# Kernel optimization log

Hardware: AMD Instinct MI355X
Metric: run time of the kernel (lower is better)

Reference implementation:

```python
import jax, jax.numpy as jnp
import numpy as np

HEADS = 4
DIM_HEAD = 32


def setup_inputs() -> dict:
    key = jax.random.key(0)
    k1, k2, k3 = jax.random.split(key, 3)
    B, L, D = 16, 8192, 256
    hidden = HEADS * DIM_HEAD  # 128
    x = jax.random.normal(k1, (B, L, D), dtype=jnp.float32)
    W_qkv = jax.random.normal(k2, (D, 3 * hidden), dtype=jnp.float32) * (D ** -0.5)
    W_out = jax.random.normal(k3, (hidden, D), dtype=jnp.float32) * (hidden ** -0.5)
    b_out = jnp.zeros((D,), dtype=jnp.float32)
    return {"x": x, "W_qkv": W_qkv, "W_out": W_out, "b_out": b_out}


def reference(x, W_qkv, W_out, b_out):
    B, L, D = x.shape
    scale = DIM_HEAD ** -0.5
    # 1x1 conv == per-token matmul
    qkv = jnp.einsum('bld,df->blf', x, W_qkv)  # [B, L, 3*h*dh]
    qkv = qkv.reshape(B, L, 3, HEADS, DIM_HEAD)
    q = jnp.transpose(qkv[:, :, 0], (0, 2, 1, 3)) * scale          # [B, h, L, d]
    k = jax.nn.softmax(jnp.transpose(qkv[:, :, 1], (0, 2, 1, 3)), axis=2)  # softmax over L
    v = jnp.transpose(qkv[:, :, 2], (0, 2, 1, 3))                  # [B, h, L, e]
    context = jnp.einsum('bhld,bhle->bhde', k, v)                  # [B, h, d, e]
    out = jnp.einsum('bhde,bhld->bhle', context, q)                # [B, h, L, e]
    out = jnp.transpose(out, (0, 2, 1, 3)).reshape(B, L, HEADS * DIM_HEAD)
    return jnp.einsum('blf,fd->bld', out, W_out) + b_out
```

## Files before the change

kernel.cpp:

```cpp
#include <hip/hip_runtime.h>
#include <math.h>


#define BL 131072

typedef __attribute__((ext_vector_type(8))) short bf16x8;
typedef __attribute__((ext_vector_type(4))) float f32x4;
typedef __attribute__((ext_vector_type(4))) unsigned u32x4;

__device__ __forceinline__ unsigned cvt_pk2(float a, float b) {
    unsigned r;
    asm("v_cvt_pk_bf16_f32 %0, %1, %2" : "=v"(r) : "v"(a), "v"(b));
    return r;
}
__device__ __forceinline__ ushort bf16_rn(float f) {
    return (ushort)cvt_pk2(f, f);
}
__device__ __forceinline__ float bf16f(ushort h) { return __uint_as_float(((unsigned)h) << 16); }

__device__ __forceinline__ void glds16(const void* g, void* l) {
    __builtin_amdgcn_global_load_lds((const __attribute__((address_space(1))) unsigned int*)g,
                                     (__attribute__((address_space(3))) unsigned int*)l,
                                     16, 0, 0);
}

__global__ __launch_bounds__(256) void init_stats(float* S, float* Z) {
    int i = blockIdx.x * 256 + threadIdx.x;
    if (i < 65536) S[i] = 0.f;
    if (i < 2048) Z[i] = 0.f;
}

__global__ __launch_bounds__(256) void convert_w(const float* __restrict__ W,
                                                 ushort* __restrict__ wh,
                                                 ushort* __restrict__ wl) {
    int n = blockIdx.x, k = threadIdx.x;
    float f = W[k * 384 + n];
    ushort h = bf16_rn(f);
    wh[n * 256 + k] = h;
    wl[n * 256 + k] = bf16_rn(f - bf16f(h));
}

__global__ __launch_bounds__(256) void gemm1_kernel(
    const float* __restrict__ X,
    const ushort* __restrict__ Wh, const ushort* __restrict__ Wl,
    ushort* __restrict__ Qh, ushort* __restrict__ Ql,
    float* __restrict__ KV) {
    __shared__ __align__(16) float  As[4096];
    __shared__ __align__(16) ushort Bsh[4096];
    __shared__ __align__(16) ushort Bsl[4096];
    const int tid = threadIdx.x;
    const int wg = blockIdx.x;
    const int xcd = wg & 7;
    const int slot = wg >> 3;
    const int cb = slot % 3;
    const int yb = (slot / 3) * 8 + xcd;
    const int col0 = cb * 128;
    const int row0 = yb * 128;
    const int lane = tid & 63, wave = tid >> 6;
    const int wr = (wave & 1) * 64, wc = (wave >> 1) * 64;
    const int m = lane & 15, quad = lane >> 4;
    const int ra = lane >> 3, pa = lane & 7;
    const int rb = lane >> 2, pb = lane & 3;

    f32x4 acc[4][4] = {};

    for (int k0 = 0; k0 < 256; k0 += 32) {
#pragma unroll
        for (int s = 0; s < 4; ++s) {
            int seg = s * 4 + wave;
            int r = seg * 8 + ra;
            int q = pa ^ (r & 7);
            glds16(&X[(long)(row0 + r) * 256 + k0 + q * 4], &As[seg * 256]);
        }
#pragma unroll
        for (int s = 0; s < 2; ++s) {
            int seg = s * 4 + wave;
            int r = seg * 16 + rb;
            int q = pb ^ ((r >> 1) & 3);
            glds16(&Wh[(long)(col0 + r) * 256 + k0 + q * 8], &Bsh[seg * 512]);
            glds16(&Wl[(long)(col0 + r) * 256 + k0 + q * 8], &Bsl[seg * 512]);
        }
        __syncthreads();

        bf16x8 bh[4], bl[4];
#pragma unroll
        for (int i = 0; i < 4; ++i) {
            int r = wc + i * 16 + m;
            int p = quad ^ ((r >> 1) & 3);
            bh[i] = *(const bf16x8*)&Bsh[r * 32 + p * 8];
            bl[i] = *(const bf16x8*)&Bsl[r * 32 + p * 8];
        }
#pragma unroll
        for (int i = 0; i < 4; ++i) {
            int r = wr + i * 16 + m;
            int p0 = (quad * 2) ^ (r & 7);
            int p1 = (quad * 2 + 1) ^ (r & 7);
            f32x4 a0 = *(const f32x4*)&As[r * 32 + p0 * 4];
            f32x4 a1 = *(const f32x4*)&As[r * 32 + p1 * 4];
            u32x4 ahw, alw;
#pragma unroll
            for (int e = 0; e < 2; ++e) {
                float f0 = a0[2 * e], f1 = a0[2 * e + 1];
                unsigned h = cvt_pk2(f0, f1);
                ahw[e] = h;
                alw[e] = cvt_pk2(f0 - __uint_as_float(h << 16),
                                 f1 - __uint_as_float(h & 0xFFFF0000u));
            }
#pragma unroll
            for (int e = 0; e < 2; ++e) {
                float f0 = a1[2 * e], f1 = a1[2 * e + 1];
                unsigned h = cvt_pk2(f0, f1);
                ahw[2 + e] = h;
                alw[2 + e] = cvt_pk2(f0 - __uint_as_float(h << 16),
                                     f1 - __uint_as_float(h & 0xFFFF0000u));
            }
            bf16x8 ah = __builtin_bit_cast(bf16x8, ahw);
            bf16x8 al = __builtin_bit_cast(bf16x8, alw);
#pragma unroll
            for (int j = 0; j < 4; ++j) {
                acc[i][j] = __builtin_amdgcn_mfma_f32_16x16x32_bf16(ah, bh[j], acc[i][j], 0, 0, 0);
                acc[i][j] = __builtin_amdgcn_mfma_f32_16x16x32_bf16(ah, bl[j], acc[i][j], 0, 0, 0);
                acc[i][j] = __builtin_amdgcn_mfma_f32_16x16x32_bf16(al, bh[j], acc[i][j], 0, 0, 0);
            }
        }
        __syncthreads();
    }

    if (cb == 0) {
#pragma unroll
        for (int i = 0; i < 4; ++i)
#pragma unroll
            for (int r4 = 0; r4 < 4; ++r4) {
                long row = row0 + wr + i * 16 + quad * 4 + r4;
#pragma unroll
                for (int j = 0; j < 4; ++j) {
                    float v = acc[i][j][r4];
                    int col = wc + j * 16 + m;
                    ushort h = bf16_rn(v);
                    Qh[row * 128 + col] = h;
                    Ql[row * 128 + col] = bf16_rn(v - bf16f(h));
                }
            }
    } else {
        int vofs = (cb == 2) ? 32 : 0;
#pragma unroll
        for (int i = 0; i < 4; ++i)
#pragma unroll
            for (int r4 = 0; r4 < 4; ++r4) {
                long row = row0 + wr + i * 16 + quad * 4 + r4;
                long b = row >> 13, l = row & 8191;
#pragma unroll
                for (int j = 0; j < 4; ++j) {
                    int c = wc + j * 16 + m;
                    int h = c >> 5, dd = c & 31;
                    KV[(((b * 4 + h) * 8192 + l) * 64) + vofs + dd] = acc[i][j][r4];
                }
            }
    }
}

__global__ __launch_bounds__(256) void ksum_hb(const float* __restrict__ KV,
                                               float* __restrict__ S,
                                               float* __restrict__ Z) {
    int bx = blockIdx.x;
    int c = bx & 7, bh = bx >> 3;
    const float* slab = KV + ((long)bh * 8192 + c * 1024) * 64;
    __shared__ float tile[64][68];
    const int tid = threadIdx.x;
    const int dcol = tid & 31;
    const int e0 = (tid >> 5) * 4;
    const int c4 = tid & 15, lrow = tid >> 4;
    float z = 0.f;
    f32x4 acc = {0.f, 0.f, 0.f, 0.f};

    for (int t0 = 0; t0 < 1024; t0 += 64) {
#pragma unroll
        for (int u = 0; u < 4; ++u) {
            int l = u * 16 + lrow;
            float4 w = *(const float4*)&slab[((long)(t0 + l)) * 64 + c4 * 4];
            if (c4 < 8) { w.x = __expf(w.x); w.y = __expf(w.y); w.z = __expf(w.z); w.w = __expf(w.w); }
            *(float4*)&tile[l][c4 * 4] = w;
        }
        __syncthreads();
#pragma unroll 8
        for (int l = 0; l < 64; ++l) {
            float e = tile[l][dcol];
            f32x4 vv = *(const f32x4*)&tile[l][32 + e0];
            z += e;
            acc[0] += e * vv[0]; acc[1] += e * vv[1];
            acc[2] += e * vv[2]; acc[3] += e * vv[3];
        }
        __syncthreads();
    }
    if (tid < 32) atomicAdd(&Z[bh * 32 + dcol], z);
#pragma unroll
    for (int j = 0; j < 4; ++j)
        atomicAdd(&S[((long)bh * 32 + dcol) * 32 + e0 + j], acc[j]);
}

__global__ __launch_bounds__(256) void combine_kernel(const float* __restrict__ S,
                                                      const float* __restrict__ Z,
                                                      const float* __restrict__ Wout,
                                                      ushort* __restrict__ m2h,
                                                      ushort* __restrict__ m2l) {
    int bh = blockIdx.x;
    int b = bh >> 2, h = bh & 3;
    int n = threadIdx.x;
    __shared__ float ctx[32][32];
    __shared__ float zs[32];
    if (n < 32) zs[n] = Z[bh * 32 + n];
    __syncthreads();
#pragma unroll
    for (int t = 0; t < 4; ++t) {
        int idx = t * 256 + n;
        int d = idx >> 5, e = idx & 31;
        ctx[d][e] = S[(long)bh * 1024 + idx] / zs[d];
    }
    __syncthreads();
    const float scale = 0.17677669529663687f;
    float acc[32];
#pragma unroll
    for (int d = 0; d < 32; ++d) acc[d] = 0.f;
    for (int e = 0; e < 32; ++e) {
        float w = Wout[(h * 32 + e) * 256 + n];
#pragma unroll
        for (int d = 0; d < 32; ++d) acc[d] += ctx[d][e] * w;
    }
#pragma unroll
    for (int d = 0; d < 32; ++d) {
        float v = acc[d] * scale;
        long idx = ((long)(b * 256 + n)) * 128 + h * 32 + d;
        ushort hh = bf16_rn(v);
        m2h[idx] = hh;
        m2l[idx] = bf16_rn(v - bf16f(hh));
    }
}

__global__ __launch_bounds__(256) void gemm2_kernel(
    const ushort* __restrict__ Ahp, const ushort* __restrict__ Alp,
    const ushort* __restrict__ Bhp, const ushort* __restrict__ Blp,
    const float* __restrict__ bias, float* __restrict__ out) {
    __shared__ __align__(16) ushort Ash[4096];
    __shared__ __align__(16) ushort Asl[4096];
    __shared__ __align__(16) ushort Bsh[4096];
    __shared__ __align__(16) ushort Bsl[4096];
    const int tid = threadIdx.x;
    const int col0 = blockIdx.x * 128;
    const int row0 = blockIdx.y * 128;
    const long bz = blockIdx.z;
    const ushort* Ah = Ahp + bz * (8192L * 128);
    const ushort* Al = Alp + bz * (8192L * 128);
    const ushort* Bh = Bhp + bz * (256L * 128);
    const ushort* Bl = Blp + bz * (256L * 128);
    const int lane = tid & 63, wave = tid >> 6;
    const int wr = (wave & 1) * 64, wc = (wave >> 1) * 64;
    const int m = lane & 15, quad = lane >> 4;
    const int rb = lane >> 2, pb = lane & 3;

    f32x4 acc[4][4] = {};

    for (int k0 = 0; k0 < 128; k0 += 32) {
#pragma unroll
        for (int s = 0; s < 2; ++s) {
            int seg = s * 4 + wave;
            int r = seg * 16 + rb;
            int q = pb ^ ((r >> 1) & 3);
            glds16(&Ah[(long)(row0 + r) * 128 + k0 + q * 8], &Ash[seg * 512]);
            glds16(&Al[(long)(row0 + r) * 128 + k0 + q * 8], &Asl[seg * 512]);
            glds16(&Bh[(long)(col0 + r) * 128 + k0 + q * 8], &Bsh[seg * 512]);
            glds16(&Bl[(long)(col0 + r) * 128 + k0 + q * 8], &Bsl[seg * 512]);
        }
        __syncthreads();

        bf16x8 af[2][4], bg[2][4];
#pragma unroll
        for (int i = 0; i < 4; ++i) {
            int rA = wr + i * 16 + m;
            int pA = quad ^ ((rA >> 1) & 3);
            af[0][i] = *(const bf16x8*)&Ash[rA * 32 + pA * 8];
            af[1][i] = *(const bf16x8*)&Asl[rA * 32 + pA * 8];
            int rB = wc + i * 16 + m;
            int pB = quad ^ ((rB >> 1) & 3);
            bg[0][i] = *(const bf16x8*)&Bsh[rB * 32 + pB * 8];
            bg[1][i] = *(const bf16x8*)&Bsl[rB * 32 + pB * 8];
        }
#pragma unroll
        for (int i = 0; i < 4; ++i)
#pragma unroll
            for (int j = 0; j < 4; ++j) {
                acc[i][j] = __builtin_amdgcn_mfma_f32_16x16x32_bf16(af[0][i], bg[0][j], acc[i][j], 0, 0, 0);
                acc[i][j] = __builtin_amdgcn_mfma_f32_16x16x32_bf16(af[0][i], bg[1][j], acc[i][j], 0, 0, 0);
                acc[i][j] = __builtin_amdgcn_mfma_f32_16x16x32_bf16(af[1][i], bg[0][j], acc[i][j], 0, 0, 0);
            }
        __syncthreads();
    }

    float bv[4];
#pragma unroll
    for (int j = 0; j < 4; ++j) bv[j] = bias[col0 + wc + j * 16 + m];
    float* outb = out + bz * (8192L * 256);
#pragma unroll
    for (int i = 0; i < 4; ++i)
#pragma unroll
        for (int r4 = 0; r4 < 4; ++r4) {
            long row = row0 + wr + i * 16 + quad * 4 + r4;
#pragma unroll
            for (int j = 0; j < 4; ++j)
                outb[row * 256 + col0 + wc + j * 16 + m] = acc[i][j][r4] + bv[j];
        }
}

extern "C" void kernel_launch(void* const* d_in, const int* in_sizes, int n_in,
                              void* d_out, int out_size, void* d_ws, size_t ws_size,
                              hipStream_t stream) {
    const float* x     = (const float*)d_in[0];
    const float* W_qkv = (const float*)d_in[1];
    const float* W_out = (const float*)d_in[2];
    const float* b_out = (const float*)d_in[3];
    float* out = (float*)d_out;

    char* p = (char*)d_ws;
    float* kv   = (float*)p;  p += (long)64 * 8192 * 64 * 4;
    float* S    = (float*)p;  p += 65536 * 4;
    float* Z    = (float*)p;  p += 2048 * 4;
    ushort* wth = (ushort*)p; p += 384 * 256 * 2;
    ushort* wtl = (ushort*)p; p += 384 * 256 * 2;
    ushort* qh  = (ushort*)p; p += (long)BL * 128 * 2;
    ushort* ql  = (ushort*)p; p += (long)BL * 128 * 2;
    ushort* m2h = (ushort*)p; p += 16 * 256 * 128 * 2;
    ushort* m2l = (ushort*)p; p += 16 * 256 * 128 * 2;

    init_stats<<<264, 256, 0, stream>>>(S, Z);
    convert_w<<<384, 256, 0, stream>>>(W_qkv, wth, wtl);

    gemm1_kernel<<<3072, 256, 0, stream>>>(x, wth, wtl, qh, ql, kv);

    ksum_hb<<<512, 256, 0, stream>>>(kv, S, Z);
    combine_kernel<<<64, 256, 0, stream>>>(S, Z, W_out, m2h, m2l);

    gemm2_kernel<<<dim3(2, 64, 16), 256, 0, stream>>>(qh, ql, m2h, m2l, b_out, out);
}
```

Before: 431.3 us.

## Double-buffer both GEMMs, register-tile ksum, merge prep kernels, swizzle gemm2 grid

Both MFMA GEMM kernels now use two LDS buffers, so the global-to-LDS loads for the next K tile are issued while the current tile is computed. The ksum reduction is reworked so each thread accumulates a 4x8 block of the context over an 8-row slice, using vector LDS reads, a padded tile layout, cross-lane shuffle reductions and fewer atomics. The stats-zeroing and weight-conversion kernels are merged into one launch. gemm2 gets a 1D grid with XCD-aware block remapping. The costs are doubled shared memory, which may reduce occupancy, and higher register pressure in ksum.

```diff
diff --git a/kernel.cpp b/kernel.cpp
--- a/kernel.cpp
+++ b/kernel.cpp
@@ -24,20 +24,19 @@
                                      16, 0, 0);
 }
 
-__global__ __launch_bounds__(256) void init_stats(float* S, float* Z) {
-    int i = blockIdx.x * 256 + threadIdx.x;
-    if (i < 65536) S[i] = 0.f;
-    if (i < 2048) Z[i] = 0.f;
-}
-
-__global__ __launch_bounds__(256) void convert_w(const float* __restrict__ W,
-                                                 ushort* __restrict__ wh,
-                                                 ushort* __restrict__ wl) {
+__global__ __launch_bounds__(256) void prep_kernel(const float* __restrict__ W,
+                                                   ushort* __restrict__ wh,
+                                                   ushort* __restrict__ wl,
+                                                   float* __restrict__ S,
+                                                   float* __restrict__ Z) {
     int n = blockIdx.x, k = threadIdx.x;
     float f = W[k * 384 + n];
     ushort h = bf16_rn(f);
     wh[n * 256 + k] = h;
     wl[n * 256 + k] = bf16_rn(f - bf16f(h));
+    int i = n * 256 + k;
+    if (i < 65536) S[i] = 0.f;
+    if (i < 2048) Z[i] = 0.f;
 }
 
 __global__ __launch_bounds__(256) void gemm1_kernel(
@@ -45,9 +44,9 @@
     const ushort* __restrict__ Wh, const ushort* __restrict__ Wl,
     ushort* __restrict__ Qh, ushort* __restrict__ Ql,
     float* __restrict__ KV) {
-    __shared__ __align__(16) float  As[4096];
-    __shared__ __align__(16) ushort Bsh[4096];
-    __shared__ __align__(16) ushort Bsl[4096];
+    __shared__ __align__(16) float  As[2][4096];
+    __shared__ __align__(16) ushort Bsh[2][4096];
+    __shared__ __align__(16) ushort Bsl[2][4096];
     const int tid = threadIdx.x;
     const int wg = blockIdx.x;
     const int xcd = wg & 7;
@@ -64,39 +63,46 @@
 
     f32x4 acc[4][4] = {};
 
-    for (int k0 = 0; k0 < 256; k0 += 32) {
+    auto STAGE = [&](int buf, int k0) {
 #pragma unroll
         for (int s = 0; s < 4; ++s) {
             int seg = s * 4 + wave;
             int r = seg * 8 + ra;
             int q = pa ^ (r & 7);
-            glds16(&X[(long)(row0 + r) * 256 + k0 + q * 4], &As[seg * 256]);
+            glds16(&X[(long)(row0 + r) * 256 + k0 + q * 4], &As[buf][seg * 256]);
         }
 #pragma unroll
         for (int s = 0; s < 2; ++s) {
             int seg = s * 4 + wave;
             int r = seg * 16 + rb;
             int q = pb ^ ((r >> 1) & 3);
-            glds16(&Wh[(long)(col0 + r) * 256 + k0 + q * 8], &Bsh[seg * 512]);
-            glds16(&Wl[(long)(col0 + r) * 256 + k0 + q * 8], &Bsl[seg * 512]);
-        }
-        __syncthreads();
+            glds16(&Wh[(long)(col0 + r) * 256 + k0 + q * 8], &Bsh[buf][seg * 512]);
+            glds16(&Wl[(long)(col0 + r) * 256 + k0 + q * 8], &Bsl[buf][seg * 512]);
+        }
+    };
+
+    STAGE(0, 0);
+    __syncthreads();
+
+    for (int kt = 0; kt < 8; ++kt) {
+        const int cur = kt & 1;
+        if (kt < 7) STAGE(cur ^ 1, (kt + 1) * 32);
 
         bf16x8 bh[4], bl[4];
 #pragma unroll
         for (int i = 0; i < 4; ++i) {
             int r = wc + i * 16 + m;
             int p = quad ^ ((r >> 1) & 3);
-            bh[i] = *(const bf16x8*)&Bsh[r * 32 + p * 8];
-            bl[i] = *(const bf16x8*)&Bsl[r * 32 + p * 8];
+            bh[i] = *(const bf16x8*)&Bsh[cur][r * 32 + p * 8];
+            bl[i] = *(const bf16x8*)&Bsl[cur][r * 32 + p * 8];
         }
 #pragma unroll
         for (int i = 0; i < 4; ++i) {
             int r = wr + i * 16 + m;
             int p0 = (quad * 2) ^ (r & 7);
             int p1 = (quad * 2 + 1) ^ (r & 7);
-            f32x4 a0 = *(const f32x4*)&As[r * 32 + p0 * 4];
-            f32x4 a1 = *(const f32x4*)&As[r * 32 + p1 * 4];
+            f32x4 a0 = *(const f32x4*)&As[cur][r * 32 + p0 * 4];
+            f32x4 a1 = *(const f32x4*)&As[cur][r * 32 + p1 * 4];
             u32x4 ahw, alw;
 #pragma unroll
             for (int e = 0; e < 2; ++e) {
@@ -163,39 +169,70 @@
                                                float* __restrict__ S,
                                                float* __restrict__ Z) {
     int bx = blockIdx.x;
-    int c = bx & 7, bh = bx >> 3;
-    const float* slab = KV + ((long)bh * 8192 + c * 1024) * 64;
-    __shared__ float tile[64][68];
+    int chunk = bx & 7, bh = bx >> 3;
+    const float* slab = KV + ((long)bh * 8192 + chunk * 1024) * 64;
+    __shared__ float tile[4128];
     const int tid = threadIdx.x;
-    const int dcol = tid & 31;
-    const int e0 = (tid >> 5) * 4;
+    const int w = tid >> 6, lane = tid & 63;
+    const int lg = lane >> 3, cc = lane & 7;
+    const int combo = w * 8 + cc;
+    const int d0 = (combo >> 2) * 4;
+    const int e0 = (combo & 3) * 8;
     const int c4 = tid & 15, lrow = tid >> 4;
-    float z = 0.f;
-    f32x4 acc = {0.f, 0.f, 0.f, 0.f};
+    float z4[4] = {0.f, 0.f, 0.f, 0.f};
+    float acc[4][8] = {};
 
     for (int t0 = 0; t0 < 1024; t0 += 64) {
 #pragma unroll
         for (int u = 0; u < 4; ++u) {
             int l = u * 16 + lrow;
-            float4 w = *(const float4*)&slab[((long)(t0 + l)) * 64 + c4 * 4];
-            if (c4 < 8) { w.x = __expf(w.x); w.y = __expf(w.y); w.z = __expf(w.z); w.w = __expf(w.w); }
-            *(float4*)&tile[l][c4 * 4] = w;
+            float4 wv = *(const float4*)&slab[((long)(t0 + l)) * 64 + c4 * 4];
+            if (c4 < 8) { wv.x = __expf(wv.x); wv.y = __expf(wv.y); wv.z = __expf(wv.z); wv.w = __expf(wv.w); }
+            *(float4*)&tile[l * 64 + (l >> 3) * 4 + c4 * 4] = wv;
         }
         __syncthreads();
-#pragma unroll 8
-        for (int l = 0; l < 64; ++l) {
-            float e = tile[l][dcol];
-            f32x4 vv = *(const f32x4*)&tile[l][32 + e0];
-            z += e;
-            acc[0] += e * vv[0]; acc[1] += e * vv[1];
-            acc[2] += e * vv[2]; acc[3] += e * vv[3];
+#pragma unroll
+        for (int j = 0; j < 8; ++j) {
+            int l = lg * 8 + j;
+            int base = l * 64 + lg * 4;
+            f32x4 ev = *(const f32x4*)&tile[base + d0];
+            f32x4 v0 = *(const f32x4*)&tile[base + 32 + e0];
+            f32x4 v1 = *(const f32x4*)&tile[base + 36 + e0];
+#pragma unroll
+            for (int q = 0; q < 4; ++q) {
+                float e = ev[q];
+                z4[q] += e;
+                acc[q][0] += e * v0[0]; acc[q][1] += e * v0[1];
+                acc[q][2] += e * v0[2]; acc[q][3] += e * v0[3];
+                acc[q][4] += e * v1[0]; acc[q][5] += e * v1[1];
+                acc[q][6] += e * v1[2]; acc[q][7] += e * v1[3];
+            }
         }
         __syncthreads();
     }
-    if (tid < 32) atomicAdd(&Z[bh * 32 + dcol], z);
-#pragma unroll
-    for (int j = 0; j < 4; ++j)
-        atomicAdd(&S[((long)bh * 32 + dcol) * 32 + e0 + j], acc[j]);
+#pragma unroll
+    for (int q = 0; q < 4; ++q) {
+        z4[q] += __shfl_xor(z4[q], 8);
+        z4[q] += __shfl_xor(z4[q], 16);
+        z4[q] += __shfl_xor(z4[q], 32);
+#pragma unroll
+        for (int j = 0; j < 8; ++j) {
+            acc[q][j] += __shfl_xor(acc[q][j], 8);
+            acc[q][j] += __shfl_xor(acc[q][j], 16);
+            acc[q][j] += __shfl_xor(acc[q][j], 32);
+        }
+    }
+    if (lg == 0) {
+#pragma unroll
+        for (int q = 0; q < 4; ++q)
+#pragma unroll
+            for (int j = 0; j < 8; ++j)
+                atomicAdd(&S[((long)bh * 32 + d0 + q) * 32 + e0 + j], acc[q][j]);
+        if ((cc & 3) == 0)
+#pragma unroll
+            for (int q = 0; q < 4; ++q)
+                atomicAdd(&Z[bh * 32 + d0 + q], z4[q]);
+    }
 }
 
 __global__ __launch_bounds__(256) void combine_kernel(const float* __restrict__ S,
@@ -240,14 +277,19 @@
     const ushort* __restrict__ Ahp, const ushort* __restrict__ Alp,
     const ushort* __restrict__ Bhp, const ushort* __restrict__ Blp,
     const float* __restrict__ bias, float* __restrict__ out) {
-    __shared__ __align__(16) ushort Ash[4096];
-    __shared__ __align__(16) ushort Asl[4096];
-    __shared__ __align__(16) ushort Bsh[4096];
-    __shared__ __align__(16) ushort Bsl[4096];
+    __shared__ __align__(16) ushort Ash[2][4096];
+    __shared__ __align__(16) ushort Asl[2][4096];
+    __shared__ __align__(16) ushort Bsh[2][4096];
+    __shared__ __align__(16) ushort Bsl[2][4096];
     const int tid = threadIdx.x;
-    const int col0 = blockIdx.x * 128;
-    const int row0 = blockIdx.y * 128;
-    const long bz = blockIdx.z;
+    const int bid = blockIdx.x;
+    const int xcd = bid & 7;
+    const int u = bid >> 3;
+    const int cbl = u & 1;
+    const int id = (u >> 1) * 8 + xcd;
+    const int col0 = cbl * 128;
+    const int row0 = (id & 63) * 128;
+    const long bz = id >> 6;
     const ushort* Ah = Ahp + bz * (8192L * 128);
     const ushort* Al = Alp + bz * (8192L * 128);
     const ushort* Bh = Bhp + bz * (256L * 128);
@@ -259,30 +301,37 @@
 
     f32x4 acc[4][4] = {};
 
-    for (int k0 = 0; k0 < 128; k0 += 32) {
+    auto STAGE = [&](int buf, int k0) {
 #pragma unroll
         for (int s = 0; s < 2; ++s) {
             int seg = s * 4 + wave;
             int r = seg * 16 + rb;
             int q = pb ^ ((r >> 1) & 3);
-            glds16(&Ah[(long)(row0 + r) * 128 + k0 + q * 8], &Ash[seg * 512]);
-            glds16(&Al[(long)(row0 + r) * 128 + k0 + q * 8], &Asl[seg * 512]);
-            glds16(&Bh[(long)(col0 + r) * 128 + k0 + q * 8], &Bsh[seg * 512]);
-            glds16(&Bl[(long)(col0 + r) * 128 + k0 + q * 8], &Bsl[seg * 512]);
-        }
-        __syncthreads();
+            glds16(&Ah[(long)(row0 + r) * 128 + k0 + q * 8], &Ash[buf][seg * 512]);
+            glds16(&Al[(long)(row0 + r) * 128 + k0 + q * 8], &Asl[buf][seg * 512]);
+            glds16(&Bh[(long)(col0 + r) * 128 + k0 + q * 8], &Bsh[buf][seg * 512]);
+            glds16(&Bl[(long)(col0 + r) * 128 + k0 + q * 8], &Bsl[buf][seg * 512]);
+        }
+    };
+
+    STAGE(0, 0);
+    __syncthreads();
+
+    for (int kt = 0; kt < 4; ++kt) {
+        const int cur = kt & 1;
+        if (kt < 3) STAGE(cur ^ 1, (kt + 1) * 32);
 
         bf16x8 af[2][4], bg[2][4];
 #pragma unroll
         for (int i = 0; i < 4; ++i) {
             int rA = wr + i * 16 + m;
             int pA = quad ^ ((rA >> 1) & 3);
-            af[0][i] = *(const bf16x8*)&Ash[rA * 32 + pA * 8];
-            af[1][i] = *(const bf16x8*)&Asl[rA * 32 + pA * 8];
+            af[0][i] = *(const bf16x8*)&Ash[cur][rA * 32 + pA * 8];
+            af[1][i] = *(const bf16x8*)&Asl[cur][rA * 32 + pA * 8];
             int rB = wc + i * 16 + m;
             int pB = quad ^ ((rB >> 1) & 3);
-            bg[0][i] = *(const bf16x8*)&Bsh[rB * 32 + pB * 8];
-            bg[1][i] = *(const bf16x8*)&Bsl[rB * 32 + pB * 8];
+            bg[0][i] = *(const bf16x8*)&Bsh[cur][rB * 32 + pB * 8];
+            bg[1][i] = *(const bf16x8*)&Bsl[cur][rB * 32 + pB * 8];
         }
 #pragma unroll
         for (int i = 0; i < 4; ++i)
@@ -330,13 +379,12 @@
     ushort* m2h = (ushort*)p; p += 16 * 256 * 128 * 2;
     ushort* m2l = (ushort*)p; p += 16 * 256 * 128 * 2;
 
-    init_stats<<<264, 256, 0, stream>>>(S, Z);
-    convert_w<<<384, 256, 0, stream>>>(W_qkv, wth, wtl);
+    prep_kernel<<<384, 256, 0, stream>>>(W_qkv, wth, wtl, S, Z);
 
     gemm1_kernel<<<3072, 256, 0, stream>>>(x, wth, wtl, qh, ql, kv);
 
     ksum_hb<<<512, 256, 0, stream>>>(kv, S, Z);
     combine_kernel<<<64, 256, 0, stream>>>(S, Z, W_out, m2h, m2l);
 
-    gemm2_kernel<<<dim3(2, 64, 16), 256, 0, stream>>>(qh, ql, m2h, m2l, b_out, out);
-}
+    gemm2_kernel<<<2048, 256, 0, stream>>>(qh, ql, m2h, m2l, b_out, out);
+}
```

Measured after the change: 429.0 us. About the same (-0.5%).
